# Kernel tuning notes

Hardware: AMD Instinct MI355X
Metric: run time of the kernel (lower is better)

## Reference

```python
import jax, jax.numpy as jnp
import numpy as np

B, C_IN, H, W = 4, 128, 32, 128   # W must equal out_channels (fc_out acts on last dim)
C_OUT, NUM_HEADS = 128, 2
BN_EPS = 1e-5


def setup_inputs() -> dict:
    key = jax.random.key(0)
    ks = jax.random.split(key, 14)
    s = 0.05  # small init scale for weights
    d = {
        "x": jax.random.normal(ks[0], (B, C_IN, H, W), jnp.float32),
        "wq": jax.random.normal(ks[1], (C_OUT, C_IN), jnp.float32) * s,
        "bq": jax.random.normal(ks[2], (C_OUT,), jnp.float32) * s,
        "wk": jax.random.normal(ks[3], (C_OUT, C_IN), jnp.float32) * s,
        "bk": jax.random.normal(ks[4], (C_OUT,), jnp.float32) * s,
        "wv": jax.random.normal(ks[5], (C_OUT, C_IN), jnp.float32) * s,
        "bv": jax.random.normal(ks[6], (C_OUT,), jnp.float32) * s,
        "fc_w": jax.random.normal(ks[7], (C_OUT, C_OUT), jnp.float32) * s,
        "fc_b": jax.random.normal(ks[8], (C_OUT,), jnp.float32) * s,
        "bn_gamma": jnp.ones((C_OUT,), jnp.float32),
        "bn_beta": jnp.zeros((C_OUT,), jnp.float32),
        "bn_mean": jax.random.normal(ks[9], (C_OUT,), jnp.float32) * 0.1,
        "bn_var": jax.random.uniform(ks[10], (C_OUT,), jnp.float32, 0.5, 1.5),
        "prelu_a": jnp.full((1,), 0.25, jnp.float32),
    }
    return d


def reference(x, wq, bq, wk, bk, wv, bv, fc_w, fc_b,
              bn_gamma, bn_beta, bn_mean, bn_var, prelu_a):
    b, c_in, h, w = x.shape
    c_out = wq.shape[0]
    nh = NUM_HEADS
    dk = c_out // nh
    L = h * w
    xf = x.reshape(b, c_in, L)                                # (B, Cin, L)
    # 1x1 convs == per-token linear projections
    q = jnp.einsum('oi,bil->bol', wq, xf) + bq[:, None]       # (B, Cout, L)
    k = jnp.einsum('oi,bil->bol', wk, xf) + bk[:, None]
    v = jnp.einsum('oi,bil->bol', wv, xf) + bv[:, None]
    Q = q.reshape(b, nh, dk, L)                               # (B, h, d_k, L)
    K = k.reshape(b, nh, dk, L)
    V = v.reshape(b, nh, dk, L)
    # scaled dot-product attention over the L = H*W tokens
    scores = jnp.einsum('bhdl,bhdm->bhlm', Q, K) / jnp.sqrt(jnp.float32(dk))
    attn = jax.nn.softmax(scores, axis=-1)                    # (B, h, L, L)
    out = jnp.einsum('bhlm,bhdm->bhdl', attn, V)              # (B, h, d_k, L)
    out = out.reshape(b, c_out, h, w)                         # (B, Cout, H, W)
    # fc_out: torch Linear on the LAST dim (W == Cout)
    y = jnp.einsum('bchw,ow->bcho', out, fc_w) + fc_b         # (B, Cout, H, W)
    # BatchNorm2d (eval mode: running stats) over channel dim
    inv = jax.lax.rsqrt(bn_var + BN_EPS)
    y = (y - bn_mean[None, :, None, None]) * (inv * bn_gamma)[None, :, None, None] \
        + bn_beta[None, :, None, None]
    # PReLU (single shared slope); dropout is identity in eval
    y = jnp.where(y > 0, y, prelu_a[0] * y)
    return y
```

## Files before the change

### kernel.cpp

```cpp
#include <hip/hip_runtime.h>

typedef _Float16 f16x8 __attribute__((ext_vector_type(8)));
typedef _Float16 f16x4t __attribute__((ext_vector_type(4)));
typedef __fp16 h16x2 __attribute__((ext_vector_type(2)));
typedef float f32x4 __attribute__((ext_vector_type(4)));
typedef float f32x16 __attribute__((ext_vector_type(16)));
typedef unsigned int uint2v __attribute__((ext_vector_type(2)));

#define L_SZ 4096

__device__ __forceinline__ unsigned short f2h(float f) {
    _Float16 h = (_Float16)f;
    return __builtin_bit_cast(unsigned short, h);
}
__device__ __forceinline__ unsigned int pk2(float a, float b) {
    h16x2 p = __builtin_amdgcn_cvt_pkrtz(a, b);
    return __builtin_bit_cast(unsigned int, p);
}
__device__ __forceinline__ float fexp2(float x) {
#if __has_builtin(__builtin_amdgcn_exp2f)
    return __builtin_amdgcn_exp2f(x);
#else
    return exp2f(x);
#endif
}
__device__ __forceinline__ float frcp(float x) {
#if __has_builtin(__builtin_amdgcn_rcpf)
    return __builtin_amdgcn_rcpf(x);
#else
    return 1.0f / x;
#endif
}
__device__ __forceinline__ void async16(unsigned short* lds, const unsigned short* g) {
    __builtin_amdgcn_global_load_lds(
        (const __attribute__((address_space(1))) unsigned int*)g,
        (__attribute__((address_space(3))) unsigned int*)lds, 16, 0, 0);
}

#define SLOT(row, ci) ((((ci) * 64) + ((row) & 32) + (((row) & 31) ^ (ci))) * 8)

__global__ __launch_bounds__(256) void prep_kernel(
    const float* __restrict__ wq, const float* __restrict__ wk,
    const float* __restrict__ wv, const float* __restrict__ fcw,
    unsigned short* __restrict__ Wimg, unsigned short* __restrict__ Fimg)
{
    int e2 = blockIdx.x * 256 + threadIdx.x;
    if (e2 < 24576) {
        const float* src = (e2 < 8192) ? wq : (e2 < 16384 ? wk : wv);
        float2 v = *(const float2*)&src[(e2 * 2) & 16383];
        int e = e2 * 2;
        int o = e >> 7, ci = (e & 127) >> 3, j = e & 7;
        *(unsigned int*)&Wimg[o * 128 + ((ci ^ (o & 15)) * 8) + j] = pk2(v.x, v.y);
    } else {
        int fe = (e2 - 24576) * 2;
        float2 v = *(const float2*)&fcw[fe];
        int o = fe >> 7, ci = (fe & 127) >> 3, j = fe & 7;
        *(unsigned int*)&Fimg[o * 128 + ((ci ^ (o & 15)) * 8) + j] = pk2(v.x, v.y);
    }
}

__global__ __launch_bounds__(256, 3) void qkv_kernel(
    const float* __restrict__ x,
    const unsigned short* __restrict__ Wimg,
    const float* __restrict__ bq, const float* __restrict__ bk,
    const float* __restrict__ bv,
    unsigned short* __restrict__ Qp, unsigned short* __restrict__ Kp,
    unsigned short* __restrict__ Vp)
{
    int raw = blockIdx.x;
    int v = (raw & 7) * 96 + (raw >> 3);
    int tile = v / 3;
    int p = v - tile * 3;
    int bidx = tile >> 6;
    int l0 = (tile & 63) * 64;
    int tid = threadIdx.x;
    int wave = tid >> 6, lane = tid & 63;
    int c = lane & 15, qd = lane >> 4;

    __shared__ __align__(16) unsigned short Ws[128 * 128];
    __shared__ __align__(16) unsigned short Sc[9216];

    const unsigned short* wsrc = Wimg + p * 16384;
    #pragma unroll
    for (int t = 0; t < 8; ++t)
        async16(&Ws[(t * 256 + wave * 64) * 8], &wsrc[(size_t)(t * 256 + wave * 64 + lane) * 8]);

    unsigned short* Xs = Sc;
    #pragma unroll
    for (int it = 0; it < 8; ++it) {
        int i  = (tid >> 4) + 16 * it;
        int l4 = (tid & 15) * 4;
        const float4 vx = *(const float4*)&x[(bidx * 128 + i) * L_SZ + l0 + l4];
        float vv[4] = {vx.x, vx.y, vx.z, vx.w};
        int ci = i >> 3;
        #pragma unroll
        for (int u = 0; u < 4; ++u) {
            int l = l4 + u;
            Xs[l * 128 + ((ci ^ (l & 15)) * 8) + (i & 7)] = f2h(vv[u]);
        }
    }
    __syncthreads();

    f16x8 afrag[4];
    #pragma unroll
    for (int kc = 0; kc < 4; ++kc) {
        int l = wave * 16 + c;
        int ci = kc * 4 + qd;
        afrag[kc] = *(const f16x8*)&Xs[l * 128 + ((ci ^ (l & 15)) * 8)];
    }
    __syncthreads();

    f32x4 acc[8];
    #pragma unroll
    for (int nt = 0; nt < 8; ++nt) acc[nt] = (f32x4){0.f, 0.f, 0.f, 0.f};

    #pragma unroll
    for (int kc = 0; kc < 4; ++kc) {
        #pragma unroll
        for (int nt = 0; nt < 8; ++nt) {
            int o = nt * 16 + c;
            f16x8 bfrag = *(const f16x8*)&Ws[o * 128 + (((kc * 4 + qd) ^ c) * 8)];
            acc[nt] = __builtin_amdgcn_mfma_f32_16x16x32_f16(afrag[kc], bfrag, acc[nt], 0, 0, 0);
        }
    }

    const float s_q = 0.18033688011f;
    if (p < 2) {
        const float* bias = (p == 0) ? bq : bk;
        unsigned short* Ot = Sc;
        #pragma unroll
        for (int nt = 0; nt < 8; ++nt) {
            int o = nt * 16 + c;
            float bo = bias[o];
            #pragma unroll
            for (int r = 0; r < 4; ++r) {
                int ll = wave * 16 + qd * 4 + r;
                float val = acc[nt][r] + bo;
                if (p == 0) val *= s_q;
                Ot[ll * 144 + o] = f2h(val);
            }
        }
        __syncthreads();
        unsigned short* dst = (p == 0) ? Qp : Kp;
        #pragma unroll
        for (int t = 0; t < 4; ++t) {
            int u = tid + t * 256;
            int row = u >> 4, col = (u & 15) * 8;
            int h = col >> 6, d = col & 63;
            uint4 a = *(const uint4*)&Ot[row * 144 + col];
            *(uint4*)&dst[((size_t)(bidx * 2 + h) * L_SZ + l0 + row) * 64 + d] = a;
        }
    } else {
        unsigned short* Vt = Sc;
        #pragma unroll
        for (int nt = 0; nt < 8; ++nt) {
            int o = nt * 16 + c;
            #pragma unroll
            for (int r = 0; r < 4; ++r) {
                int ll = wave * 16 + qd * 4 + r;
                Vt[o * 72 + ll] = f2h(acc[nt][r] + bv[o]);
            }
        }
        __syncthreads();
        #pragma unroll
        for (int t = 0; t < 2; ++t) {
            int u = tid + t * 256;
            int row = u >> 2;
            int lc = (u & 3) * 16;
            uint4 a0 = *(const uint4*)&Vt[row * 72 + lc];
            uint4 a1 = *(const uint4*)&Vt[row * 72 + lc + 8];
            *(uint4*)&Vp[(size_t)(bidx * 128 + row) * L_SZ + l0 + lc] = a0;
            *(uint4*)&Vp[(size_t)(bidx * 128 + row) * L_SZ + l0 + lc + 8] = a1;
        }
    }
}

__global__ __launch_bounds__(256, 4) void attn_kernel(
    const unsigned short* __restrict__ Qp, const unsigned short* __restrict__ Kp,
    const unsigned short* __restrict__ Vp,
    unsigned short* __restrict__ Opart, float* __restrict__ Mpart, float* __restrict__ Lpart)
{
    int raw = blockIdx.x;
    int blk = (raw & 7) * 128 + (raw >> 3);
    int lt = blk & 31;
    int bh = (blk >> 5) & 7;
    int sp = blk >> 8;
    int l0 = lt * 128;
    int tid = threadIdx.x;
    int wave = tid >> 6, lane = tid & 63;
    int ln = lane & 31, hi = lane >> 5;
    int b = bh >> 1, h = bh & 1;

    __shared__ __align__(16) unsigned short Ks[2][4096];
    __shared__ __align__(16) unsigned short Vs[3][4096];

    const unsigned short* Qb = Qp + (size_t)bh * L_SZ * 64;
    const unsigned short* Kb = Kp + (size_t)bh * L_SZ * 64;
    const unsigned short* Vb = Vp + ((size_t)b * 128 + h * 64) * L_SZ;

    int lq = l0 + wave * 32 + ln;
    f16x8 qf[4];
    #pragma unroll
    for (int kc = 0; kc < 4; ++kc)
        qf[kc] = *(const f16x8*)&Qb[(size_t)lq * 64 + kc * 16 + hi * 8];

    float m_st = -1e30f, lsum = 0.f;
    f32x16 acc0 = {}, acc1 = {};
    uint4 pp[4];

    int mglob = sp * 1024;
    int ci0 = wave, ci1 = 4 + wave;
    int r0_ = (lane & 32) | ((lane & 31) ^ ci0);
    int r1_ = (lane & 32) | ((lane & 31) ^ ci1);

#define STAGEK(t, kb) do {                                                        \
        int m0_ = mglob + (t) * 64;                                               \
        async16(&Ks[kb][(wave * 64) * 8],       &Kb[(size_t)(m0_ + r0_) * 64 + ci0 * 8]); \
        async16(&Ks[kb][(256 + wave * 64) * 8], &Kb[(size_t)(m0_ + r1_) * 64 + ci1 * 8]); \
    } while (0)
#define STAGEV(t, vb) do {                                                        \
        int m0_ = mglob + (t) * 64;                                               \
        async16(&Vs[vb][(wave * 64) * 8],       &Vb[(size_t)r0_ * L_SZ + m0_ + ci0 * 8]); \
        async16(&Vs[vb][(256 + wave * 64) * 8], &Vb[(size_t)r1_ * L_SZ + m0_ + ci1 * 8]); \
    } while (0)

#define QK_COMPUTE(kb) do {                                                       \
        s0 = (f32x16){}; s1 = (f32x16){};                                         \
        _Pragma("unroll")                                                         \
        for (int kc = 0; kc < 4; ++kc) {                                          \
            int cd = kc * 2 + hi;                                                 \
            f16x8 k0 = *(const f16x8*)&Ks[kb][SLOT(ln, cd)];                      \
            f16x8 k1 = *(const f16x8*)&Ks[kb][SLOT(32 + ln, cd)];                 \
            s0 = __builtin_amdgcn_mfma_f32_32x32x16_f16(k0, qf[kc], s0, 0, 0, 0); \
            s1 = __builtin_amdgcn_mfma_f32_32x32x16_f16(k1, qf[kc], s1, 0, 0, 0); \
        }                                                                         \
    } while (0)

#define PV_ACC(vb) do {                                                           \
        const unsigned short* Vsl = &Vs[vb][0];                                   \
        _Pragma("unroll")                                                         \
        for (int kc = 0; kc < 4; ++kc) {                                          \
            f16x8 pf = __builtin_bit_cast(f16x8, pp[kc]);                         \
            int cd = kc * 2 + hi;                                                 \
            f16x8 v0 = *(const f16x8*)&Vsl[SLOT(ln, cd)];                         \
            f16x8 v1 = *(const f16x8*)&Vsl[SLOT(32 + ln, cd)];                    \
            acc0 = __builtin_amdgcn_mfma_f32_32x32x16_f16(v0, pf, acc0, 0, 0, 0); \
            acc1 = __builtin_amdgcn_mfma_f32_32x32x16_f16(v1, pf, acc1, 0, 0, 0); \
        }                                                                         \
    } while (0)

#define SOFTMAX_PACK() do {                                                       \
        float t_[8];                                                              \
        _Pragma("unroll")                                                         \
        for (int r = 0; r < 8; ++r)                                               \
            t_[r] = fmaxf(fmaxf(s0[r], s0[r + 8]), s1[r]);                        \
        _Pragma("unroll")                                                         \
        for (int r = 0; r < 4; ++r)                                               \
            t_[r] = fmaxf(fmaxf(t_[r], t_[r + 4]), s1[8 + r]);                    \
        float m01 = fmaxf(fmaxf(t_[0], t_[1]), s1[12]);                           \
        float m23 = fmaxf(fmaxf(t_[2], t_[3]), s1[13]);                           \
        float mx = fmaxf(fmaxf(m01, m23), fmaxf(s1[14], s1[15]));                 \
        mx = fmaxf(mx, __shfl_xor(mx, 32));                                       \
        if (!__all(mx <= m_st + 8.0f)) {                                          \
            float mnew = fmaxf(m_st, mx);                                         \
            float alpha = fexp2(m_st - mnew);                                     \
            m_st = mnew;                                                          \
            lsum *= alpha;                                                        \
            _Pragma("unroll")                                                     \
            for (int r = 0; r < 16; ++r) { acc0[r] *= alpha; acc1[r] *= alpha; }  \
        }                                                                         \
        float rs0 = 0.f, rs1 = 0.f, rs2 = 0.f, rs3 = 0.f;                         \
        _Pragma("unroll")                                                         \
        for (int r = 0; r < 4; ++r) {                                             \
            float p0 = fexp2(s0[r]      - m_st); s0[r]      = p0; rs0 += p0;      \
            float p1 = fexp2(s0[r + 4]  - m_st); s0[r + 4]  = p1; rs1 += p1;      \
            float p2 = fexp2(s0[r + 8]  - m_st); s0[r + 8]  = p2; rs2 += p2;      \
            float p3 = fexp2(s0[r + 12] - m_st); s0[r + 12] = p3; rs3 += p3;      \
        }                                                                         \
        _Pragma("unroll")                                                         \
        for (int r = 0; r < 4; ++r) {                                             \
            float p0 = fexp2(s1[r]      - m_st); s1[r]      = p0; rs0 += p0;      \
            float p1 = fexp2(s1[r + 4]  - m_st); s1[r + 4]  = p1; rs1 += p1;      \
            float p2 = fexp2(s1[r + 8]  - m_st); s1[r + 8]  = p2; rs2 += p2;      \
            float p3 = fexp2(s1[r + 12] - m_st); s1[r + 12] = p3; rs3 += p3;      \
        }                                                                         \
        lsum += (rs0 + rs1) + (rs2 + rs3);                                        \
        _Pragma("unroll")                                                         \
        for (int kc = 0; kc < 4; ++kc) {                                          \
            unsigned int a0, a1, a2, a3;                                          \
            if (kc == 0) {                                                        \
                a0 = pk2(s0[0], s0[1]);  a1 = pk2(s0[2], s0[3]);                  \
                a2 = pk2(s0[4], s0[5]);  a3 = pk2(s0[6], s0[7]);                  \
            } else if (kc == 1) {                                                 \
                a0 = pk2(s0[8], s0[9]);  a1 = pk2(s0[10], s0[11]);                \
                a2 = pk2(s0[12], s0[13]); a3 = pk2(s0[14], s0[15]);               \
            } else if (kc == 2) {                                                 \
                a0 = pk2(s1[0], s1[1]);  a1 = pk2(s1[2], s1[3]);                  \
                a2 = pk2(s1[4], s1[5]);  a3 = pk2(s1[6], s1[7]);                  \
            } else {                                                              \
                a0 = pk2(s1[8], s1[9]);  a1 = pk2(s1[10], s1[11]);                \
                a2 = pk2(s1[12], s1[13]); a3 = pk2(s1[14], s1[15]);               \
            }                                                                     \
            uint2v r02 = __builtin_amdgcn_permlane32_swap(a0, a2, false, false);  \
            uint2v r13 = __builtin_amdgcn_permlane32_swap(a1, a3, false, false);  \
            uint4 pw; pw.x = r02[0]; pw.y = r13[0]; pw.z = r02[1]; pw.w = r13[1]; \
            pp[kc] = pw;                                                          \
        }                                                                         \
    } while (0)

    f32x16 s0, s1;

    STAGEK(0, 0); STAGEV(0, 0);
    __syncthreads();
    STAGEK(1, 1); STAGEV(1, 1);
    __builtin_amdgcn_s_setprio(1);
    QK_COMPUTE(0);
    SOFTMAX_PACK();
    __builtin_amdgcn_s_setprio(0);

    for (int t = 1; t < 16; ++t) {
        __syncthreads();
        if (t < 15) { STAGEK(t + 1, (t + 1) & 1); STAGEV(t + 1, (t + 1) % 3); }

        __builtin_amdgcn_s_setprio(1);
        QK_COMPUTE(t & 1);
        PV_ACC((t - 1) % 3);
        SOFTMAX_PACK();
        __builtin_amdgcn_s_setprio(0);
    }
    __builtin_amdgcn_s_setprio(1);
    PV_ACC(0);
    __builtin_amdgcn_s_setprio(0);

#undef STAGEK
#undef STAGEV
#undef QK_COMPUTE
#undef PV_ACC
#undef SOFTMAX_PACK

    float l_tot = lsum + __shfl_xor(lsum, 32);
    unsigned short* Ow = Opart + (size_t)(sp * 8 + bh) * 64 * 4096;
    #pragma unroll
    for (int r = 0; r < 16; ++r) {
        int d0 = (r & 3) + 8 * (r >> 2) + 4 * hi;
        Ow[(size_t)d0 * 4096 + lq] = f2h(acc0[r]);
        Ow[(size_t)(32 + d0) * 4096 + lq] = f2h(acc1[r]);
    }
    if (hi == 0) {
        Mpart[(sp * 8 + bh) * 4096 + lq] = m_st;
        Lpart[(sp * 8 + bh) * 4096 + lq] = l_tot;
    }
}

__global__ __launch_bounds__(256) void scl_kernel(
    const float* __restrict__ Mp, const float* __restrict__ Lp,
    unsigned short* __restrict__ SclImg)
{
    int gid = blockIdx.x * 256 + threadIdx.x;
    int bh = gid >> 12, l = gid & 4095;
    float m0 = Mp[(0 * 8 + bh) * 4096 + l], m1 = Mp[(1 * 8 + bh) * 4096 + l];
    float m2 = Mp[(2 * 8 + bh) * 4096 + l], m3 = Mp[(3 * 8 + bh) * 4096 + l];
    float mx = fmaxf(fmaxf(m0, m1), fmaxf(m2, m3));
    float a0 = fexp2(m0 - mx), a1 = fexp2(m1 - mx);
    float a2 = fexp2(m2 - mx), a3 = fexp2(m3 - mx);
    float den = a0 * Lp[(0 * 8 + bh) * 4096 + l] + a1 * Lp[(1 * 8 + bh) * 4096 + l]
              + a2 * Lp[(2 * 8 + bh) * 4096 + l] + a3 * Lp[(3 * 8 + bh) * 4096 + l];
    float inv = frcp(den);
    int hl = l >> 7, ww = l & 127;
    int slot = hl * 128 + ((ww + hl) & 127);
    uint2 sc;
    sc.x = pk2(a0 * inv, a1 * inv);
    sc.y = pk2(a2 * inv, a3 * inv);
    *(uint2*)&SclImg[((size_t)bh * 4096 + slot) * 4] = sc;
}

__global__ __launch_bounds__(256, 2) void fc_kernel(
    const unsigned short* __restrict__ Opart,
    const unsigned short* __restrict__ SclImg,
    const unsigned short* __restrict__ Fimg,
    const float* __restrict__ fc_b, const float* __restrict__ bn_g,
    const float* __restrict__ bn_b, const float* __restrict__ bn_m,
    const float* __restrict__ bn_v, const float* __restrict__ prelu_a,
    float* __restrict__ out)
{
    int raw = blockIdx.x;
    int blk = (raw & 7) * 64 + (raw >> 3);
    int r0 = blk * 32;
    int tid = threadIdx.x;
    int c0 = blk & 127;
    int bh = blk >> 6;
    int d = c0 & 63;

    int wave = tid >> 6, lane = tid & 63;
    int c = lane & 15, qd = lane >> 4;
    int rw = r0 + (wave >> 1) * 16;
    int o0 = (wave & 1) * 64;
    int hh = (rw + c) & 31;

    __shared__ __align__(16) unsigned short Fw[128 * 128];
    __shared__ __align__(16) unsigned short SclU[4096 * 4];

    #pragma unroll
    for (int t = 0; t < 8; ++t)
        async16(&SclU[(t * 256 + wave * 64) * 8],
                &SclImg[(size_t)bh * 16384 + (size_t)(t * 256 + wave * 64 + lane) * 8]);
    #pragma unroll
    for (int t = 0; t < 8; ++t)
        async16(&Fw[(t * 256 + wave * 64) * 8],
                &Fimg[(size_t)(t * 256 + wave * 64 + lane) * 8]);

    uint4 ovr[4][4];
    #pragma unroll
    for (int kc = 0; kc < 4; ++kc) {
        int w0 = kc * 32 + qd * 8;
        #pragma unroll
        for (int s = 0; s < 4; ++s)
            ovr[kc][s] = *(const uint4*)&Opart[(size_t)(s * 8 + bh) * 262144 + (size_t)d * 4096 + hh * 128 + w0];
    }
    __syncthreads();

    f16x8 af[4];
    #pragma unroll
    for (int kc = 0; kc < 4; ++kc) {
        int w0 = kc * 32 + qd * 8;
        f16x8 ov0 = __builtin_bit_cast(f16x8, ovr[kc][0]);
        f16x8 ov1 = __builtin_bit_cast(f16x8, ovr[kc][1]);
        f16x8 ov2 = __builtin_bit_cast(f16x8, ovr[kc][2]);
        f16x8 ov3 = __builtin_bit_cast(f16x8, ovr[kc][3]);
        #pragma unroll
        for (int j = 0; j < 8; ++j) {
            int slot = hh * 128 + ((w0 + j + hh) & 127);
            f16x4t sc = *(const f16x4t*)&SclU[slot * 4];
            float v = (float)ov0[j] * (float)sc[0] + (float)ov1[j] * (float)sc[1]
                    + (float)ov2[j] * (float)sc[2] + (float)ov3[j] * (float)sc[3];
            af[kc][j] = (_Float16)v;
        }
    }

    f32x4 acc[4];
    #pragma unroll
    for (int nt = 0; nt < 4; ++nt) acc[nt] = (f32x4){0.f, 0.f, 0.f, 0.f};
    #pragma unroll
    for (int kc = 0; kc < 4; ++kc) {
        #pragma unroll
        for (int nt = 0; nt < 4; ++nt) {
            int o = o0 + nt * 16 + c;
            f16x8 bf = *(const f16x8*)&Fw[o * 128 + (((kc * 4 + qd) ^ c) * 8)];
            acc[nt] = __builtin_amdgcn_mfma_f32_16x16x32_f16(af[kc], bf, acc[nt], 0, 0, 0);
        }
    }

    float pa = prelu_a[0];
    float g  = bn_g[c0] * rsqrtf(bn_v[c0] + 1e-5f);
    float mn = bn_m[c0], bt = bn_b[c0];
    #pragma unroll
    for (int r = 0; r < 4; ++r) {
        int orow = rw + qd * 4 + r;
        #pragma unroll
        for (int nt = 0; nt < 4; ++nt) {
            int o = o0 + nt * 16 + c;
            float y = (acc[nt][r] + fc_b[o] - mn) * g + bt;
            y = y > 0.f ? y : pa * y;
            out[(size_t)orow * 128 + o] = y;
        }
    }
}

extern "C" void kernel_launch(void* const* d_in, const int* in_sizes, int n_in,
                              void* d_out, int out_size, void* d_ws, size_t ws_size,
                              hipStream_t stream) {
    const float* x     = (const float*)d_in[0];
    const float* wq    = (const float*)d_in[1];
    const float* bq    = (const float*)d_in[2];
    const float* wk    = (const float*)d_in[3];
    const float* bk    = (const float*)d_in[4];
    const float* wv    = (const float*)d_in[5];
    const float* bv    = (const float*)d_in[6];
    const float* fcw_f = (const float*)d_in[7];
    const float* fcb   = (const float*)d_in[8];
    const float* bn_g  = (const float*)d_in[9];
    const float* bn_b  = (const float*)d_in[10];
    const float* bn_m  = (const float*)d_in[11];
    const float* bn_v  = (const float*)d_in[12];
    const float* pa    = (const float*)d_in[13];
    float* out = (float*)d_out;

    unsigned short* Qp  = (unsigned short*)d_ws;
    unsigned short* Kp  = Qp + 8 * L_SZ * 64;
    unsigned short* Vp  = Kp + 8 * L_SZ * 64;
    unsigned short* Opart = Vp + 8 * L_SZ * 64;
    float* Mpart = (float*)(Opart + 4 * 8 * 64 * L_SZ);
    float* Lpart = Mpart + 4 * 8 * L_SZ;
    unsigned short* Wimg   = (unsigned short*)(Lpart + 4 * 8 * L_SZ);
    unsigned short* Fimg   = Wimg + 384 * 128;
    unsigned short* SclImg = Fimg + 128 * 128;

    hipLaunchKernelGGL(prep_kernel, dim3(128),  dim3(256), 0, stream,
                       wq, wk, wv, fcw_f, Wimg, Fimg);
    hipLaunchKernelGGL(qkv_kernel,  dim3(768),  dim3(256), 0, stream,
                       x, Wimg, bq, bk, bv, Qp, Kp, Vp);
    hipLaunchKernelGGL(attn_kernel, dim3(1024), dim3(256), 0, stream,
                       Qp, Kp, Vp, Opart, Mpart, Lpart);
    hipLaunchKernelGGL(scl_kernel,  dim3(128),  dim3(256), 0, stream,
                       Mpart, Lpart, SclImg);
    hipLaunchKernelGGL(fc_kernel,   dim3(512),  dim3(256), 0, stream,
                       Opart, SclImg, Fimg, fcb, bn_g, bn_b, bn_m, bn_v, pa, out);
}
```

Before: 167.9 us.

## Collapse deferred PV pipeline into same-iteration PV and double-buffer V

```diff
diff --git a/kernel.cpp b/kernel.cpp
--- a/kernel.cpp
+++ b/kernel.cpp
@@ -192,7 +192,7 @@
     int b = bh >> 1, h = bh & 1;
 
     __shared__ __align__(16) unsigned short Ks[2][4096];
-    __shared__ __align__(16) unsigned short Vs[3][4096];
+    __shared__ __align__(16) unsigned short Vs[2][4096];
 
     const unsigned short* Qb = Qp + (size_t)bh * L_SZ * 64;
     const unsigned short* Kb = Kp + (size_t)bh * L_SZ * 64;
@@ -204,24 +204,20 @@
     for (int kc = 0; kc < 4; ++kc)
         qf[kc] = *(const f16x8*)&Qb[(size_t)lq * 64 + kc * 16 + hi * 8];
 
-    float m_st = -1e30f, lsum = 0.f;
+    float m_st = 0.f, lsum = 0.f;
     f32x16 acc0 = {}, acc1 = {};
-    uint4 pp[4];
 
     int mglob = sp * 1024;
     int ci0 = wave, ci1 = 4 + wave;
     int r0_ = (lane & 32) | ((lane & 31) ^ ci0);
     int r1_ = (lane & 32) | ((lane & 31) ^ ci1);
 
-#define STAGEK(t, kb) do {                                                        \
+#define STAGE(t, buf) do {                                                        \
         int m0_ = mglob + (t) * 64;                                               \
-        async16(&Ks[kb][(wave * 64) * 8],       &Kb[(size_t)(m0_ + r0_) * 64 + ci0 * 8]); \
-        async16(&Ks[kb][(256 + wave * 64) * 8], &Kb[(size_t)(m0_ + r1_) * 64 + ci1 * 8]); \
-    } while (0)
-#define STAGEV(t, vb) do {                                                        \
-        int m0_ = mglob + (t) * 64;                                               \
-        async16(&Vs[vb][(wave * 64) * 8],       &Vb[(size_t)r0_ * L_SZ + m0_ + ci0 * 8]); \
-        async16(&Vs[vb][(256 + wave * 64) * 8], &Vb[(size_t)r1_ * L_SZ + m0_ + ci1 * 8]); \
+        async16(&Ks[buf][(wave * 64) * 8],       &Kb[(size_t)(m0_ + r0_) * 64 + ci0 * 8]); \
+        async16(&Ks[buf][(256 + wave * 64) * 8], &Kb[(size_t)(m0_ + r1_) * 64 + ci1 * 8]); \
+        async16(&Vs[buf][(wave * 64) * 8],       &Vb[(size_t)r0_ * L_SZ + m0_ + ci0 * 8]); \
+        async16(&Vs[buf][(256 + wave * 64) * 8], &Vb[(size_t)r1_ * L_SZ + m0_ + ci1 * 8]); \
     } while (0)
 
 #define QK_COMPUTE(kb) do {                                                       \
@@ -236,20 +232,7 @@
         }                                                                         \
     } while (0)
 
-#define PV_ACC(vb) do {                                                           \
-        const unsigned short* Vsl = &Vs[vb][0];                                   \
-        _Pragma("unroll")                                                         \
-        for (int kc = 0; kc < 4; ++kc) {                                          \
-            f16x8 pf = __builtin_bit_cast(f16x8, pp[kc]);                         \
-            int cd = kc * 2 + hi;                                                 \
-            f16x8 v0 = *(const f16x8*)&Vsl[SLOT(ln, cd)];                         \
-            f16x8 v1 = *(const f16x8*)&Vsl[SLOT(32 + ln, cd)];                    \
-            acc0 = __builtin_amdgcn_mfma_f32_32x32x16_f16(v0, pf, acc0, 0, 0, 0); \
-            acc1 = __builtin_amdgcn_mfma_f32_32x32x16_f16(v1, pf, acc1, 0, 0, 0); \
-        }                                                                         \
-    } while (0)
-
-#define SOFTMAX_PACK() do {                                                       \
+#define TREEMAX(mx) do {                                                          \
         float t_[8];                                                              \
         _Pragma("unroll")                                                         \
         for (int r = 0; r < 8; ++r)                                               \
@@ -259,17 +242,11 @@
             t_[r] = fmaxf(fmaxf(t_[r], t_[r + 4]), s1[8 + r]);                    \
         float m01 = fmaxf(fmaxf(t_[0], t_[1]), s1[12]);                           \
         float m23 = fmaxf(fmaxf(t_[2], t_[3]), s1[13]);                           \
-        float mx = fmaxf(fmaxf(m01, m23), fmaxf(s1[14], s1[15]));                 \
+        mx = fmaxf(fmaxf(m01, m23), fmaxf(s1[14], s1[15]));                       \
         mx = fmaxf(mx, __shfl_xor(mx, 32));                                       \
-        if (!__all(mx <= m_st + 8.0f)) {                                          \
-            float mnew = fmaxf(m_st, mx);                                         \
-            float alpha = fexp2(m_st - mnew);                                     \
-            m_st = mnew;                                                          \
-            lsum *= alpha;                                                        \
-            _Pragma("unroll")                                                     \
-            for (int r = 0; r < 16; ++r) { acc0[r] *= alpha; acc1[r] *= alpha; }  \
-        }                                                                         \
-        float rs0 = 0.f, rs1 = 0.f, rs2 = 0.f, rs3 = 0.f;                         \
+    } while (0)
+
+#define EXPS(rs0, rs1, rs2, rs3) do {                                             \
         _Pragma("unroll")                                                         \
         for (int r = 0; r < 4; ++r) {                                             \
             float p0 = fexp2(s0[r]      - m_st); s0[r]      = p0; rs0 += p0;      \
@@ -284,7 +261,9 @@
             float p2 = fexp2(s1[r + 8]  - m_st); s1[r + 8]  = p2; rs2 += p2;      \
             float p3 = fexp2(s1[r + 12] - m_st); s1[r + 12] = p3; rs3 += p3;      \
         }                                                                         \
-        lsum += (rs0 + rs1) + (rs2 + rs3);                                        \
+    } while (0)
+
+#define PACK_PV(vb) do {                                                          \
         _Pragma("unroll")                                                         \
         for (int kc = 0; kc < 4; ++kc) {                                          \
             unsigned int a0, a1, a2, a3;                                          \
@@ -304,39 +283,65 @@
             uint2v r02 = __builtin_amdgcn_permlane32_swap(a0, a2, false, false);  \
             uint2v r13 = __builtin_amdgcn_permlane32_swap(a1, a3, false, false);  \
             uint4 pw; pw.x = r02[0]; pw.y = r13[0]; pw.z = r02[1]; pw.w = r13[1]; \
-            pp[kc] = pw;                                                          \
+            f16x8 pf = __builtin_bit_cast(f16x8, pw);                             \
+            int cd = kc * 2 + hi;                                                 \
+            f16x8 v0 = *(const f16x8*)&Vs[vb][SLOT(ln, cd)];                      \
+            f16x8 v1 = *(const f16x8*)&Vs[vb][SLOT(32 + ln, cd)];                 \
+            acc0 = __builtin_amdgcn_mfma_f32_32x32x16_f16(v0, pf, acc0, 0, 0, 0); \
+            acc1 = __builtin_amdgcn_mfma_f32_32x32x16_f16(v1, pf, acc1, 0, 0, 0); \
         }                                                                         \
     } while (0)
 
     f32x16 s0, s1;
 
-    STAGEK(0, 0); STAGEV(0, 0);
+    STAGE(0, 0);
     __syncthreads();
-    STAGEK(1, 1); STAGEV(1, 1);
+    STAGE(1, 1);
     __builtin_amdgcn_s_setprio(1);
     QK_COMPUTE(0);
-    SOFTMAX_PACK();
+    {
+        float mx; TREEMAX(mx);
+        m_st = mx;
+        float rs0 = 0.f, rs1 = 0.f, rs2 = 0.f, rs3 = 0.f;
+        EXPS(rs0, rs1, rs2, rs3);
+        lsum = (rs0 + rs1) + (rs2 + rs3);
+    }
+    PACK_PV(0);
     __builtin_amdgcn_s_setprio(0);
 
     for (int t = 1; t < 16; ++t) {
+        int cur = t & 1;
         __syncthreads();
-        if (t < 15) { STAGEK(t + 1, (t + 1) & 1); STAGEV(t + 1, (t + 1) % 3); }
+        if (t < 15) STAGE(t + 1, cur ^ 1);
 
         __builtin_amdgcn_s_setprio(1);
-        QK_COMPUTE(t & 1);
-        PV_ACC((t - 1) % 3);
-        SOFTMAX_PACK();
+        QK_COMPUTE(cur);
+        {
+            float rs0 = 0.f, rs1 = 0.f, rs2 = 0.f, rs3 = 0.f;
+            float mx; TREEMAX(mx);
+            EXPS(rs0, rs1, rs2, rs3);
+            if (!__all(mx <= m_st + 8.0f)) {
+                float mnew = fmaxf(m_st, mx);
+                float alpha = fexp2(m_st - mnew);
+                m_st = mnew;
+                lsum *= alpha;
+                #pragma unroll
+                for (int r = 0; r < 16; ++r) {
+                    acc0[r] *= alpha; acc1[r] *= alpha;
+                    s0[r] *= alpha;   s1[r] *= alpha;
+                }
+                rs0 *= alpha; rs1 *= alpha; rs2 *= alpha; rs3 *= alpha;
+            }
+            lsum += (rs0 + rs1) + (rs2 + rs3);
+        }
+        PACK_PV(cur);
         __builtin_amdgcn_s_setprio(0);
     }
-    __builtin_amdgcn_s_setprio(1);
-    PV_ACC(0);
-    __builtin_amdgcn_s_setprio(0);
-
-#undef STAGEK
-#undef STAGEV
+#undef STAGE
 #undef QK_COMPUTE
-#undef PV_ACC
-#undef SOFTMAX_PACK
+#undef TREEMAX
+#undef EXPS
+#undef PACK_PV
 
     float l_tot = lsum + __shfl_xor(lsum, 32);
     unsigned short* Ow = Opart + (size_t)(sp * 8 + bh) * 64 * 4096;
```

Measured after the change: 160.2 us. -4.6%, faster.
